# Kernel tuning notes

Measured on AMD Instinct MI355X. Metric: run time of the kernel, lower is better.

## Reference

```python
import jax, jax.numpy as jnp
import numpy as np

K = 64
P = 13               # int(1 + 0.2 * K), module default
KP = K + P - 1       # truncation degree of the polynomial
N_S = 2048
N_C = 10000
NEG = -1e9           # finite stand-in for -inf (log of zero coefficient); keeps vjp NaN-free


def setup_inputs() -> dict:
    key = jax.random.key(0)
    x = jax.random.normal(key, (N_S, N_C), dtype=jnp.float32)
    return {"x": x}


def _log_esp(x, kp):
    """Log elementary symmetric polynomials of exp(x) along the class axis.

    x: (n_s, n_c). Returns L of shape (kp+1, n_s) with
    L[j, s] = log sigma_j(exp(x[s, :])), exactly the truncated log-domain
    polynomial product prod_i (1 + exp(x_i) t) that the torch module computes
    via divide-and-conquer.
    """
    n_s, n_c = x.shape
    # carry: log-coefficients of the partial product, degrees 0..kp
    init = jnp.full((kp + 1, n_s), NEG, dtype=x.dtype).at[0].set(0.0)
    pad = jnp.full((1, n_s), NEG, dtype=x.dtype)

    def step(L, xi):
        # multiply partial polynomial by (1 + exp(xi) t), truncated at degree kp
        shifted = jnp.concatenate([pad, L[:-1] + xi[None, :]], axis=0)
        return jnp.logaddexp(L, shifted), None

    L, _ = jax.lax.scan(step, init, x.T)  # scan over n_c classes
    return L


def reference(x):
    coeff = _log_esp(x, KP)          # (kp+1, n_s)
    return coeff[K - 1:K + 1]        # (2, n_s): log sigma_{k-1}, log sigma_k
```

## Files before the change

### kernel.cpp

```cpp
#include <hip/hip_runtime.h>


#define NS 2048
#define NC 10000
#define KSEL 64

__device__ __forceinline__ float4 ld4(const float* p) { return *(const float4*)p; }

__global__ __launch_bounds__(256, 4)
void logesp_kernel(const float* __restrict__ x, float* __restrict__ out) {
  __shared__ float RA[1280];
  __shared__ float RB[896];
  __shared__ float scLog[32];
  __shared__ float red[8];

  const int t  = threadIdx.x;
  const int wv = t >> 6;
  const int s  = blockIdx.x;

  float c0 = 1.f, c1 = 0.f, c2 = 0.f, c3 = 0.f, c4 = 0.f, c5 = 0.f, c6 = 0.f;
  float sw = 0.f;
  const float4* xv = (const float4*)(x + (size_t)s * NC);

#pragma unroll
  for (int it = 0; it < 9; ++it) {
    const float4 v = xv[t + it * 256];
#pragma unroll
    for (int q = 0; q < 4; ++q) {
      const float xval = q == 0 ? v.x : q == 1 ? v.y : q == 2 ? v.z : v.w;
      const float wgt = __expf(xval);
      sw += wgt;
      c6 = fmaf(wgt, c5, c6);
      c5 = fmaf(wgt, c4, c5);
      c4 = fmaf(wgt, c3, c4);
      c3 = fmaf(wgt, c2, c3);
      c2 = fmaf(wgt, c1, c2);
      c1 = fmaf(wgt, c0, c1);
    }
  }
  if (t < 196) {
    const float4 v = xv[2304 + t];
#pragma unroll
    for (int q = 0; q < 4; ++q) {
      const float xval = q == 0 ? v.x : q == 1 ? v.y : q == 2 ? v.z : v.w;
      const float wgt = __expf(xval);
      sw += wgt;
      c6 = fmaf(wgt, c5, c6);
      c5 = fmaf(wgt, c4, c5);
      c4 = fmaf(wgt, c3, c4);
      c3 = fmaf(wgt, c2, c3);
      c2 = fmaf(wgt, c1, c2);
      c1 = fmaf(wgt, c0, c1);
    }
  }

#pragma unroll
  for (int m = 1; m < 64; m <<= 1) sw += __shfl_xor(sw, m);
  if ((t & 63) == 0) red[wv] = sw;
  if (t < 32) scLog[t] = 0.f;
  __syncthreads();
  const float wsum = red[0] + red[1] + red[2] + red[3];
  const float tau = __logf(wsum * ((float)(NC - KSEL) / ((float)KSEL * (float)NC)));

  {
    const float f1 = __expf(-tau);
    const float f2 = f1 * f1, f3 = f2 * f1, f4v = f2 * f2, f5 = f4v * f1, f6 = f4v * f2;
    c1 *= f1; c2 *= f2; c3 *= f3; c4 *= f4v; c5 *= f5; c6 *= f6;
  }
  float mx = fmaxf(fmaxf(fmaxf(c0, c1), fmaxf(c2, c3)), fmaxf(fmaxf(c4, c5), c6));
  {
    const float inv = 1.f / mx;
    c0 *= inv; c1 *= inv; c2 *= inv; c3 *= inv; c4 *= inv; c5 *= inv; c6 *= inv;
  }
  {
    float Sr = __logf(mx);
#pragma unroll
    for (int m = 1; m < 64; m <<= 1) Sr += __shfl_xor(Sr, m);
    if ((t & 63) == 0) red[4 + wv] = Sr;
  }

  const float q0 = __shfl_xor(c0, 1), q1 = __shfl_xor(c1, 1), q2 = __shfl_xor(c2, 1),
              q3 = __shfl_xor(c3, 1), q4 = __shfl_xor(c4, 1), q5 = __shfl_xor(c5, 1),
              q6 = __shfl_xor(c6, 1);
  float e0 = c0 * q0;
  float e1 = fmaf(c1, q0, c0 * q1);
  float e2 = fmaf(c2, q0, fmaf(c1, q1, c0 * q2));
  float e3 = fmaf(c3, q0, fmaf(c2, q1, fmaf(c1, q2, c0 * q3)));
  float e4 = fmaf(c4, q0, fmaf(c3, q1, fmaf(c2, q2, fmaf(c1, q3, c0 * q4))));
  float e5 = fmaf(c5, q0, fmaf(c4, q1, fmaf(c3, q2, fmaf(c2, q3, fmaf(c1, q4, c0 * q5)))));
  float e6 = fmaf(c6, q0, fmaf(c5, q1, fmaf(c4, q2, fmaf(c3, q3, fmaf(c2, q4, fmaf(c1, q5, c0 * q6))))));
  float e7 = fmaf(c6, q1, fmaf(c5, q2, fmaf(c4, q3, fmaf(c3, q4, fmaf(c2, q5, c1 * q6)))));

  const float f0 = __shfl_xor(e0, 2), f1 = __shfl_xor(e1, 2), f2 = __shfl_xor(e2, 2),
              f3 = __shfl_xor(e3, 2), f4 = __shfl_xor(e4, 2), f5 = __shfl_xor(e5, 2),
              f6 = __shfl_xor(e6, 2), f7 = __shfl_xor(e7, 2);
  const float g0 = e0 * f0;
  const float g1 = fmaf(e1, f0, e0 * f1);
  const float g2 = fmaf(e2, f0, fmaf(e1, f1, e0 * f2));
  const float g3 = fmaf(e3, f0, fmaf(e2, f1, fmaf(e1, f2, e0 * f3)));
  const float g4 = fmaf(e4, f0, fmaf(e3, f1, fmaf(e2, f2, fmaf(e1, f3, e0 * f4))));
  const float g5 = fmaf(e5, f0, fmaf(e4, f1, fmaf(e3, f2, fmaf(e2, f3, fmaf(e1, f4, e0 * f5)))));
  const float g6 = fmaf(e6, f0, fmaf(e5, f1, fmaf(e4, f2, fmaf(e3, f3, fmaf(e2, f4, fmaf(e1, f5, e0 * f6))))));
  const float g7 = fmaf(e7, f0, fmaf(e6, f1, fmaf(e5, f2, fmaf(e4, f3, fmaf(e3, f4, fmaf(e2, f5, fmaf(e1, f6, e0 * f7)))))));
  const float g8 = fmaf(e7, f1, fmaf(e6, f2, fmaf(e5, f3, fmaf(e4, f4, fmaf(e3, f5, fmaf(e2, f6, e1 * f7))))));
  const float g9 = fmaf(e7, f2, fmaf(e6, f3, fmaf(e5, f4, fmaf(e4, f5, fmaf(e3, f6, e2 * f7)))));
  const float g10 = fmaf(e7, f3, fmaf(e6, f4, fmaf(e5, f5, fmaf(e4, f6, e3 * f7))));
  const float g11 = fmaf(e7, f4, fmaf(e6, f5, fmaf(e5, f6, e4 * f7)));

  if ((t & 3) == 0) {
    float* row = RA + (t >> 2) * 20;
    *(float4*)(row)      = make_float4(0.f, 0.f, 0.f, 0.f);
    *(float4*)(row + 4)  = make_float4(g0, g1, g2, g3);
    *(float4*)(row + 8)  = make_float4(g4, g5, g6, g7);
    *(float4*)(row + 12) = make_float4(g8, g9, g10, g11);
    *(float4*)(row + 16) = make_float4(0.f, 0.f, 0.f, 0.f);
  }
  __syncthreads();

  {
    const int m = t >> 3, r = t & 7;
    const float* A = RA + (2 * m) * 20;
    const float* B = RA + (2 * m + 1) * 20;
    float a0 = 0.f, a1 = 0.f, a2 = 0.f, a3 = 0.f;
    if (r < 4) {
      const int j0 = 4 * r;
      const int imax = (j0 + 3 < 12) ? j0 + 3 : 12;
      for (int i0 = 0; i0 <= imax; i0 += 4) {
        const float4 a4 = ld4(A + 4 + i0);
        const float4 bl = ld4(B + j0 - i0);
        const float4 bh = ld4(B + 4 + j0 - i0);
        a0 = fmaf(a4.x, bh.x, a0); a1 = fmaf(a4.x, bh.y, a1); a2 = fmaf(a4.x, bh.z, a2); a3 = fmaf(a4.x, bh.w, a3);
        a0 = fmaf(a4.y, bl.w, a0); a1 = fmaf(a4.y, bh.x, a1); a2 = fmaf(a4.y, bh.y, a2); a3 = fmaf(a4.y, bh.z, a3);
        a0 = fmaf(a4.z, bl.z, a0); a1 = fmaf(a4.z, bl.w, a1); a2 = fmaf(a4.z, bh.x, a2); a3 = fmaf(a4.z, bh.y, a3);
        a0 = fmaf(a4.w, bl.y, a0); a1 = fmaf(a4.w, bl.z, a1); a2 = fmaf(a4.w, bl.w, a2); a3 = fmaf(a4.w, bh.x, a3);
      }
    }
    float m2 = fmaxf(fmaxf(a0, a1), fmaxf(a2, a3));
    m2 = fmaxf(m2, __shfl_xor(m2, 1)); m2 = fmaxf(m2, __shfl_xor(m2, 2)); m2 = fmaxf(m2, __shfl_xor(m2, 4));
    const float inv = 1.f / m2;
    float* o = RB + m * 28;
    if (r < 4) *(float4*)(o + 4 + 4 * r) = make_float4(a0 * inv, a1 * inv, a2 * inv, a3 * inv);
    if (r == 4) *(float4*)(o) = make_float4(0.f, 0.f, 0.f, 0.f);
    if (r == 5) *(float4*)(o + 20) = make_float4(0.f, 0.f, 0.f, 0.f);
    if (r == 0) scLog[m] += __logf(m2);
  }
  __syncthreads();

  {
    const int m = t >> 4, r = t & 15;
    const float* A = RB + (2 * m) * 28;
    const float* B = RB + (2 * m + 1) * 28;
    float a0 = 0.f, a1 = 0.f, a2 = 0.f, a3 = 0.f;
    if (r < 5) {
      const int j0 = 4 * r;
      const int imax = (j0 + 3 < 16) ? j0 + 3 : 16;
      for (int i0 = 0; i0 <= imax; i0 += 4) {
        const float4 a4 = ld4(A + 4 + i0);
        const float4 bl = ld4(B + j0 - i0);
        const float4 bh = ld4(B + 4 + j0 - i0);
        a0 = fmaf(a4.x, bh.x, a0); a1 = fmaf(a4.x, bh.y, a1); a2 = fmaf(a4.x, bh.z, a2); a3 = fmaf(a4.x, bh.w, a3);
        a0 = fmaf(a4.y, bl.w, a0); a1 = fmaf(a4.y, bh.x, a1); a2 = fmaf(a4.y, bh.y, a2); a3 = fmaf(a4.y, bh.z, a3);
        a0 = fmaf(a4.z, bl.z, a0); a1 = fmaf(a4.z, bl.w, a1); a2 = fmaf(a4.z, bh.x, a2); a3 = fmaf(a4.z, bh.y, a3);
        a0 = fmaf(a4.w, bl.y, a0); a1 = fmaf(a4.w, bl.z, a1); a2 = fmaf(a4.w, bl.w, a2); a3 = fmaf(a4.w, bh.x, a3);
      }
    }
    float m2 = fmaxf(fmaxf(a0, a1), fmaxf(a2, a3));
    m2 = fmaxf(m2, __shfl_xor(m2, 1)); m2 = fmaxf(m2, __shfl_xor(m2, 2));
    m2 = fmaxf(m2, __shfl_xor(m2, 4)); m2 = fmaxf(m2, __shfl_xor(m2, 8));
    const float inv = 1.f / m2;
    float* o = RA + m * 52;
    if (r < 5) *(float4*)(o + 20 + 4 * r) = make_float4(a0 * inv, a1 * inv, a2 * inv, a3 * inv);
    if (r >= 5 && r < 10) *(float4*)(o + 4 * (r - 5)) = make_float4(0.f, 0.f, 0.f, 0.f);
    if (r >= 10 && r < 13) *(float4*)(o + 40 + 4 * (r - 10)) = make_float4(0.f, 0.f, 0.f, 0.f);
    if (r == 0) scLog[m] += __logf(m2);
  }
  __syncthreads();

  {
    const int half = (t >> 5) & 1;
    const int m = 2 * wv + half;
    const int p = t & 31;
    const float* A = RA + (2 * m) * 52 + 20;
    const float* B = RA + (2 * m + 1) * 52 + 20;
    float acc = 0.f;
#pragma unroll
    for (int i0 = 0; i0 < 20; i0 += 4) {
      const float4 a4 = ld4(A + i0);
      acc = fmaf(a4.x, B[p - i0], acc);
      acc = fmaf(a4.y, B[p - i0 - 1], acc);
      acc = fmaf(a4.z, B[p - i0 - 2], acc);
      acc = fmaf(a4.w, B[p - i0 - 3], acc);
    }
    float m2 = acc;
    m2 = fmaxf(m2, __shfl_xor(m2, 1)); m2 = fmaxf(m2, __shfl_xor(m2, 2));
    m2 = fmaxf(m2, __shfl_xor(m2, 4)); m2 = fmaxf(m2, __shfl_xor(m2, 8));
    m2 = fmaxf(m2, __shfl_xor(m2, 16));
    const float inv = 1.f / m2;
    float* o = RB + m * 84;
    o[32 + p] = acc * inv;
    if (p < 8) *(float4*)(o + 4 * p) = make_float4(0.f, 0.f, 0.f, 0.f);
    if (p >= 8 && p < 13) *(float4*)(o + 64 + 4 * (p - 8)) = make_float4(0.f, 0.f, 0.f, 0.f);
    if (p == 0) scLog[m] += __logf(m2);
  }
  __syncthreads();

  {
    const int p = t & 63;
    const float* A = RB + (2 * wv) * 84 + 32;
    const float* B = RB + (2 * wv + 1) * 84 + 32;
    float acc = 0.f;
    if (p < 48) {
#pragma unroll
      for (int i0 = 0; i0 < 32; i0 += 4) {
        const float4 a4 = ld4(A + i0);
        acc = fmaf(a4.x, B[p - i0], acc);
        acc = fmaf(a4.y, B[p - i0 - 1], acc);
        acc = fmaf(a4.z, B[p - i0 - 2], acc);
        acc = fmaf(a4.w, B[p - i0 - 3], acc);
      }
    }
    float m2 = acc;
#pragma unroll
    for (int msk = 1; msk < 64; msk <<= 1) m2 = fmaxf(m2, __shfl_xor(m2, msk));
    const float inv = 1.f / m2;
    float* o = RA + wv * 116;
    if (p < 48) o[48 + p] = acc * inv;
    if (p >= 48 && p < 60) *(float4*)(o + 4 * (p - 48)) = make_float4(0.f, 0.f, 0.f, 0.f);
    if (p >= 60) *(float4*)(o + 96 + 4 * (p - 60)) = make_float4(0.f, 0.f, 0.f, 0.f);
    if (p == 59) *(float4*)(o + 112) = make_float4(0.f, 0.f, 0.f, 0.f);
    if (p == 0) scLog[wv] += __logf(m2);
  }
  __syncthreads();

  if (t < 128) {
    const int p = t & 63;
    const float* A = RA + (2 * wv) * 116 + 48;
    const float* B = RA + (2 * wv + 1) * 116 + 48;
    float acc = 0.f;
#pragma unroll
    for (int i0 = 0; i0 < 48; i0 += 4) {
      const float4 a4 = ld4(A + i0);
      acc = fmaf(a4.x, B[p - i0], acc);
      acc = fmaf(a4.y, B[p - i0 - 1], acc);
      acc = fmaf(a4.z, B[p - i0 - 2], acc);
      acc = fmaf(a4.w, B[p - i0 - 3], acc);
    }
    float c64 = (p < 48) ? A[p] * B[64 - p] : 0.f;
#pragma unroll
    for (int msk = 1; msk < 64; msk <<= 1) c64 += __shfl_xor(c64, msk);
    float m2 = fmaxf(acc, c64);
#pragma unroll
    for (int msk = 1; msk < 64; msk <<= 1) m2 = fmaxf(m2, __shfl_xor(m2, msk));
    const float inv = 1.f / m2;
    float* o = RB + wv * 76;
    o[4 + p] = acc * inv;
    if (p == 0) { o[68] = c64 * inv; scLog[wv] += __logf(m2); }
    if (p == 1) *(float4*)(o) = make_float4(0.f, 0.f, 0.f, 0.f);
  }
  __syncthreads();

  if (t < 64) {
    const float* A = RB + 4;
    const float* B = RB + 76 + 4;
    const float a = A[t];
    float v63 = a * B[63 - t];
    float v64 = a * B[64 - t];
    float ee = (t < 32) ? scLog[t] : 0.f;
#pragma unroll
    for (int msk = 1; msk < 64; msk <<= 1) {
      v63 += __shfl_xor(v63, msk);
      v64 += __shfl_xor(v64, msk);
      ee  += __shfl_xor(ee, msk);
    }
    if (t == 0) {
      v64 = fmaf(A[64], B[0], v64);
      const float Ssum = red[4] + red[5] + red[6] + red[7] + ee;
      out[s]      = __logf(v63) + Ssum + 63.f * tau;
      out[NS + s] = __logf(v64) + Ssum + 64.f * tau;
    }
  }
}

extern "C" void kernel_launch(void* const* d_in, const int* in_sizes, int n_in,
                              void* d_out, int out_size, void* d_ws, size_t ws_size,
                              hipStream_t stream) {
  const float* x = (const float*)d_in[0];
  float* out = (float*)d_out;
  (void)in_sizes; (void)n_in; (void)d_ws; (void)ws_size; (void)out_size;
  logesp_kernel<<<NS, 256, 0, stream>>>(x, out);
}
```

Before: 32.28 us.

## Drop block barriers in the tree merge by keeping each level wave-local

Restructures the polynomial-product tree so the first four merge levels each read and write only data owned by the same wavefront. This lets the __syncthreads between those levels be removed. Every level gets its own shared buffer with padded rows and a per-level scLog slot, and the convolutions become scalar-unrolled loops instead of float4 blocked ones. Global loads are all issued up front into a register buffer, with the tail padded by -1e30 instead of a branch, and launch bounds go from 4 to 5 blocks per CU. Risks are higher register pressure from the buffered loads and some extra scalar LDS reads.

```diff
diff --git a/kernel.cpp b/kernel.cpp
--- a/kernel.cpp
+++ b/kernel.cpp
@@ -5,59 +5,50 @@
 #define NC 10000
 #define KSEL 64
 
-__device__ __forceinline__ float4 ld4(const float* p) { return *(const float4*)p; }
-
-__global__ __launch_bounds__(256, 4)
+__global__ __launch_bounds__(256, 5)
 void logesp_kernel(const float* __restrict__ x, float* __restrict__ out) {
-  __shared__ float RA[1280];
-  __shared__ float RB[896];
-  __shared__ float scLog[32];
+  __shared__ float W2[64 * 28];
+  __shared__ float W3[32 * 37];
+  __shared__ float W4[16 * 53];
+  __shared__ float W5[8 * 77];
+  __shared__ float W6[4 * 109];
+  __shared__ float W7[2 * 70];
+  __shared__ float scLog[64];
   __shared__ float red[8];
 
   const int t  = threadIdx.x;
   const int wv = t >> 6;
   const int s  = blockIdx.x;
 
+  const float4* xv = (const float4*)(x + (size_t)s * NC);
+  float4 buf[10];
+#pragma unroll
+  for (int it = 0; it < 9; ++it) buf[it] = xv[t + it * 256];
+  buf[9] = make_float4(-1e30f, -1e30f, -1e30f, -1e30f);
+  if (t < 196) buf[9] = xv[2304 + t];
+
   float c0 = 1.f, c1 = 0.f, c2 = 0.f, c3 = 0.f, c4 = 0.f, c5 = 0.f, c6 = 0.f;
   float sw = 0.f;
-  const float4* xv = (const float4*)(x + (size_t)s * NC);
-
-#pragma unroll
-  for (int it = 0; it < 9; ++it) {
-    const float4 v = xv[t + it * 256];
+#pragma unroll
+  for (int it = 0; it < 10; ++it) {
+    const float4 v = buf[it];
 #pragma unroll
     for (int q = 0; q < 4; ++q) {
       const float xval = q == 0 ? v.x : q == 1 ? v.y : q == 2 ? v.z : v.w;
-      const float wgt = __expf(xval);
-      sw += wgt;
-      c6 = fmaf(wgt, c5, c6);
-      c5 = fmaf(wgt, c4, c5);
-      c4 = fmaf(wgt, c3, c4);
-      c3 = fmaf(wgt, c2, c3);
-      c2 = fmaf(wgt, c1, c2);
-      c1 = fmaf(wgt, c0, c1);
-    }
-  }
-  if (t < 196) {
-    const float4 v = xv[2304 + t];
-#pragma unroll
-    for (int q = 0; q < 4; ++q) {
-      const float xval = q == 0 ? v.x : q == 1 ? v.y : q == 2 ? v.z : v.w;
-      const float wgt = __expf(xval);
-      sw += wgt;
-      c6 = fmaf(wgt, c5, c6);
-      c5 = fmaf(wgt, c4, c5);
-      c4 = fmaf(wgt, c3, c4);
-      c3 = fmaf(wgt, c2, c3);
-      c2 = fmaf(wgt, c1, c2);
-      c1 = fmaf(wgt, c0, c1);
+      const float w = __expf(xval);
+      sw += w;
+      c6 = fmaf(w, c5, c6);
+      c5 = fmaf(w, c4, c5);
+      c4 = fmaf(w, c3, c4);
+      c3 = fmaf(w, c2, c3);
+      c2 = fmaf(w, c1, c2);
+      c1 = fmaf(w, c0, c1);
     }
   }
 
 #pragma unroll
   for (int m = 1; m < 64; m <<= 1) sw += __shfl_xor(sw, m);
   if ((t & 63) == 0) red[wv] = sw;
-  if (t < 32) scLog[t] = 0.f;
   __syncthreads();
   const float wsum = red[0] + red[1] + red[2] + red[3];
   const float tau = __logf(wsum * ((float)(NC - KSEL) / ((float)KSEL * (float)NC)));
@@ -67,12 +58,10 @@
     const float f2 = f1 * f1, f3 = f2 * f1, f4v = f2 * f2, f5 = f4v * f1, f6 = f4v * f2;
     c1 *= f1; c2 *= f2; c3 *= f3; c4 *= f4v; c5 *= f5; c6 *= f6;
   }
-  float mx = fmaxf(fmaxf(fmaxf(c0, c1), fmaxf(c2, c3)), fmaxf(fmaxf(c4, c5), c6));
-  {
-    const float inv = 1.f / mx;
-    c0 *= inv; c1 *= inv; c2 *= inv; c3 *= inv; c4 *= inv; c5 *= inv; c6 *= inv;
-  }
-  {
+  {
+    const float mx = fmaxf(fmaxf(fmaxf(c0, c1), fmaxf(c2, c3)), fmaxf(fmaxf(c4, c5), c6));
+    const float invm = 1.f / mx;
+    c0 *= invm; c1 *= invm; c2 *= invm; c3 *= invm; c4 *= invm; c5 *= invm; c6 *= invm;
     float Sr = __logf(mx);
 #pragma unroll
     for (int m = 1; m < 64; m <<= 1) Sr += __shfl_xor(Sr, m);
@@ -82,14 +71,14 @@
   const float q0 = __shfl_xor(c0, 1), q1 = __shfl_xor(c1, 1), q2 = __shfl_xor(c2, 1),
               q3 = __shfl_xor(c3, 1), q4 = __shfl_xor(c4, 1), q5 = __shfl_xor(c5, 1),
               q6 = __shfl_xor(c6, 1);
-  float e0 = c0 * q0;
-  float e1 = fmaf(c1, q0, c0 * q1);
-  float e2 = fmaf(c2, q0, fmaf(c1, q1, c0 * q2));
-  float e3 = fmaf(c3, q0, fmaf(c2, q1, fmaf(c1, q2, c0 * q3)));
-  float e4 = fmaf(c4, q0, fmaf(c3, q1, fmaf(c2, q2, fmaf(c1, q3, c0 * q4))));
-  float e5 = fmaf(c5, q0, fmaf(c4, q1, fmaf(c3, q2, fmaf(c2, q3, fmaf(c1, q4, c0 * q5)))));
-  float e6 = fmaf(c6, q0, fmaf(c5, q1, fmaf(c4, q2, fmaf(c3, q3, fmaf(c2, q4, fmaf(c1, q5, c0 * q6))))));
-  float e7 = fmaf(c6, q1, fmaf(c5, q2, fmaf(c4, q3, fmaf(c3, q4, fmaf(c2, q5, c1 * q6)))));
+  const float e0 = c0 * q0;
+  const float e1 = fmaf(c1, q0, c0 * q1);
+  const float e2 = fmaf(c2, q0, fmaf(c1, q1, c0 * q2));
+  const float e3 = fmaf(c3, q0, fmaf(c2, q1, fmaf(c1, q2, c0 * q3)));
+  const float e4 = fmaf(c4, q0, fmaf(c3, q1, fmaf(c2, q2, fmaf(c1, q3, c0 * q4))));
+  const float e5 = fmaf(c5, q0, fmaf(c4, q1, fmaf(c3, q2, fmaf(c2, q3, fmaf(c1, q4, c0 * q5)))));
+  const float e6 = fmaf(c6, q0, fmaf(c5, q1, fmaf(c4, q2, fmaf(c3, q3, fmaf(c2, q4, fmaf(c1, q5, c0 * q6))))));
+  const float e7 = fmaf(c6, q1, fmaf(c5, q2, fmaf(c4, q3, fmaf(c3, q4, fmaf(c2, q5, c1 * q6)))));
 
   const float f0 = __shfl_xor(e0, 2), f1 = __shfl_xor(e1, 2), f2 = __shfl_xor(e2, 2),
               f3 = __shfl_xor(e3, 2), f4 = __shfl_xor(e4, 2), f5 = __shfl_xor(e5, 2),
@@ -108,164 +97,144 @@
   const float g11 = fmaf(e7, f4, fmaf(e6, f5, fmaf(e5, f6, e4 * f7)));
 
   if ((t & 3) == 0) {
-    float* row = RA + (t >> 2) * 20;
+    float* row = W2 + (t >> 2) * 28;
     *(float4*)(row)      = make_float4(0.f, 0.f, 0.f, 0.f);
-    *(float4*)(row + 4)  = make_float4(g0, g1, g2, g3);
-    *(float4*)(row + 8)  = make_float4(g4, g5, g6, g7);
-    *(float4*)(row + 12) = make_float4(g8, g9, g10, g11);
-    *(float4*)(row + 16) = make_float4(0.f, 0.f, 0.f, 0.f);
-  }
-  __syncthreads();
+    *(float4*)(row + 4)  = make_float4(0.f, 0.f, 0.f, 0.f);
+    *(float4*)(row + 8)  = make_float4(0.f, 0.f, 0.f, g0);
+    *(float4*)(row + 12) = make_float4(g1, g2, g3, g4);
+    *(float4*)(row + 16) = make_float4(g5, g6, g7, g8);
+    *(float4*)(row + 20) = make_float4(g9, g10, g11, 0.f);
+    *(float4*)(row + 24) = make_float4(0.f, 0.f, 0.f, 0.f);
+  }
 
   {
     const int m = t >> 3, r = t & 7;
-    const float* A = RA + (2 * m) * 20;
-    const float* B = RA + (2 * m + 1) * 20;
-    float a0 = 0.f, a1 = 0.f, a2 = 0.f, a3 = 0.f;
-    if (r < 4) {
-      const int j0 = 4 * r;
-      const int imax = (j0 + 3 < 12) ? j0 + 3 : 12;
-      for (int i0 = 0; i0 <= imax; i0 += 4) {
-        const float4 a4 = ld4(A + 4 + i0);
-        const float4 bl = ld4(B + j0 - i0);
-        const float4 bh = ld4(B + 4 + j0 - i0);
-        a0 = fmaf(a4.x, bh.x, a0); a1 = fmaf(a4.x, bh.y, a1); a2 = fmaf(a4.x, bh.z, a2); a3 = fmaf(a4.x, bh.w, a3);
-        a0 = fmaf(a4.y, bl.w, a0); a1 = fmaf(a4.y, bh.x, a1); a2 = fmaf(a4.y, bh.y, a2); a3 = fmaf(a4.y, bh.z, a3);
-        a0 = fmaf(a4.z, bl.z, a0); a1 = fmaf(a4.z, bl.w, a1); a2 = fmaf(a4.z, bh.x, a2); a3 = fmaf(a4.z, bh.y, a3);
-        a0 = fmaf(a4.w, bl.y, a0); a1 = fmaf(a4.w, bl.z, a1); a2 = fmaf(a4.w, bl.w, a2); a3 = fmaf(a4.w, bh.x, a3);
-      }
-    }
-    float m2 = fmaxf(fmaxf(a0, a1), fmaxf(a2, a3));
-    m2 = fmaxf(m2, __shfl_xor(m2, 1)); m2 = fmaxf(m2, __shfl_xor(m2, 2)); m2 = fmaxf(m2, __shfl_xor(m2, 4));
-    const float inv = 1.f / m2;
-    float* o = RB + m * 28;
-    if (r < 4) *(float4*)(o + 4 + 4 * r) = make_float4(a0 * inv, a1 * inv, a2 * inv, a3 * inv);
-    if (r == 4) *(float4*)(o) = make_float4(0.f, 0.f, 0.f, 0.f);
-    if (r == 5) *(float4*)(o + 20) = make_float4(0.f, 0.f, 0.f, 0.f);
-    if (r == 0) scLog[m] += __logf(m2);
-  }
-  __syncthreads();
+    const float* A = W2 + (2 * m) * 28;
+    const float* B = W2 + (2 * m + 1) * 28;
+    float o0 = 0.f, o1 = 0.f, o2 = 0.f;
+#pragma unroll
+    for (int i = 0; i <= 11; ++i) {
+      const float ai = A[11 + i];
+      o0 = fmaf(ai, B[11 + r - i], o0);
+      o1 = fmaf(ai, B[19 + r - i], o1);
+      o2 = fmaf(ai, B[27 - i], o2);
+    }
+    float mx = fmaxf(fmaxf(o0, o1), o2);
+    mx = fmaxf(mx, __shfl_xor(mx, 1));
+    mx = fmaxf(mx, __shfl_xor(mx, 2));
+    mx = fmaxf(mx, __shfl_xor(mx, 4));
+    const float inv = 1.f / mx;
+    float* O = W3 + m * 37;
+    O[16 + r] = o0 * inv;
+    O[24 + r] = o1 * inv;
+    if (r == 0) { O[32] = o2 * inv; scLog[m] = __logf(mx); }
+    O[r] = 0.f; O[8 + r] = 0.f;
+    if (r < 4) O[33 + r] = 0.f;
+  }
 
   {
     const int m = t >> 4, r = t & 15;
-    const float* A = RB + (2 * m) * 28;
-    const float* B = RB + (2 * m + 1) * 28;
-    float a0 = 0.f, a1 = 0.f, a2 = 0.f, a3 = 0.f;
-    if (r < 5) {
-      const int j0 = 4 * r;
-      const int imax = (j0 + 3 < 16) ? j0 + 3 : 16;
-      for (int i0 = 0; i0 <= imax; i0 += 4) {
-        const float4 a4 = ld4(A + 4 + i0);
-        const float4 bl = ld4(B + j0 - i0);
-        const float4 bh = ld4(B + 4 + j0 - i0);
-        a0 = fmaf(a4.x, bh.x, a0); a1 = fmaf(a4.x, bh.y, a1); a2 = fmaf(a4.x, bh.z, a2); a3 = fmaf(a4.x, bh.w, a3);
-        a0 = fmaf(a4.y, bl.w, a0); a1 = fmaf(a4.y, bh.x, a1); a2 = fmaf(a4.y, bh.y, a2); a3 = fmaf(a4.y, bh.z, a3);
-        a0 = fmaf(a4.z, bl.z, a0); a1 = fmaf(a4.z, bl.w, a1); a2 = fmaf(a4.z, bh.x, a2); a3 = fmaf(a4.z, bh.y, a3);
-        a0 = fmaf(a4.w, bl.y, a0); a1 = fmaf(a4.w, bl.z, a1); a2 = fmaf(a4.w, bl.w, a2); a3 = fmaf(a4.w, bh.x, a3);
-      }
-    }
-    float m2 = fmaxf(fmaxf(a0, a1), fmaxf(a2, a3));
-    m2 = fmaxf(m2, __shfl_xor(m2, 1)); m2 = fmaxf(m2, __shfl_xor(m2, 2));
-    m2 = fmaxf(m2, __shfl_xor(m2, 4)); m2 = fmaxf(m2, __shfl_xor(m2, 8));
-    const float inv = 1.f / m2;
-    float* o = RA + m * 52;
-    if (r < 5) *(float4*)(o + 20 + 4 * r) = make_float4(a0 * inv, a1 * inv, a2 * inv, a3 * inv);
-    if (r >= 5 && r < 10) *(float4*)(o + 4 * (r - 5)) = make_float4(0.f, 0.f, 0.f, 0.f);
-    if (r >= 10 && r < 13) *(float4*)(o + 40 + 4 * (r - 10)) = make_float4(0.f, 0.f, 0.f, 0.f);
-    if (r == 0) scLog[m] += __logf(m2);
-  }
-  __syncthreads();
-
-  {
-    const int half = (t >> 5) & 1;
-    const int m = 2 * wv + half;
-    const int p = t & 31;
-    const float* A = RA + (2 * m) * 52 + 20;
-    const float* B = RA + (2 * m + 1) * 52 + 20;
-    float acc = 0.f;
-#pragma unroll
-    for (int i0 = 0; i0 < 20; i0 += 4) {
-      const float4 a4 = ld4(A + i0);
-      acc = fmaf(a4.x, B[p - i0], acc);
-      acc = fmaf(a4.y, B[p - i0 - 1], acc);
-      acc = fmaf(a4.z, B[p - i0 - 2], acc);
-      acc = fmaf(a4.w, B[p - i0 - 3], acc);
-    }
-    float m2 = acc;
-    m2 = fmaxf(m2, __shfl_xor(m2, 1)); m2 = fmaxf(m2, __shfl_xor(m2, 2));
-    m2 = fmaxf(m2, __shfl_xor(m2, 4)); m2 = fmaxf(m2, __shfl_xor(m2, 8));
-    m2 = fmaxf(m2, __shfl_xor(m2, 16));
-    const float inv = 1.f / m2;
-    float* o = RB + m * 84;
-    o[32 + p] = acc * inv;
-    if (p < 8) *(float4*)(o + 4 * p) = make_float4(0.f, 0.f, 0.f, 0.f);
-    if (p >= 8 && p < 13) *(float4*)(o + 64 + 4 * (p - 8)) = make_float4(0.f, 0.f, 0.f, 0.f);
-    if (p == 0) scLog[m] += __logf(m2);
-  }
-  __syncthreads();
+    const float* A = W3 + (2 * m) * 37;
+    const float* B = W3 + (2 * m + 1) * 37;
+    float o0 = 0.f, o1 = 0.f;
+#pragma unroll
+    for (int i = 0; i <= 16; ++i) {
+      const float ai = A[16 + i];
+      o0 = fmaf(ai, B[16 + r - i], o0);
+      o1 = fmaf(ai, B[32 + r - i], o1);
+    }
+    if (r >= 5) o1 = 0.f;
+    float mx = fmaxf(o0, o1);
+    mx = fmaxf(mx, __shfl_xor(mx, 1));
+    mx = fmaxf(mx, __shfl_xor(mx, 2));
+    mx = fmaxf(mx, __shfl_xor(mx, 4));
+    mx = fmaxf(mx, __shfl_xor(mx, 8));
+    const float inv = 1.f / mx;
+    float* O = W4 + m * 53;
+    O[20 + r] = o0 * inv;
+    if (r < 5) O[36 + r] = o1 * inv;
+    if (r == 0) scLog[32 + m] = __logf(mx);
+    O[r] = 0.f;
+    if (r < 4) O[16 + r] = 0.f;
+    if (r < 12) O[41 + r] = 0.f;
+  }
+
+  {
+    const int m = t >> 5, p = t & 31;
+    const float* A = W4 + (2 * m) * 53;
+    const float* B = W4 + (2 * m + 1) * 53;
+    float o0 = 0.f, o1 = 0.f;
+#pragma unroll
+    for (int i = 0; i <= 20; ++i) {
+      const float ai = A[20 + i];
+      o0 = fmaf(ai, B[20 + p - i], o0);
+      o1 = fmaf(ai, B[52 - i], o1);
+    }
+    float mx = fmaxf(o0, o1);
+    mx = fmaxf(mx, __shfl_xor(mx, 1));
+    mx = fmaxf(mx, __shfl_xor(mx, 2));
+    mx = fmaxf(mx, __shfl_xor(mx, 4));
+    mx = fmaxf(mx, __shfl_xor(mx, 8));
+    mx = fmaxf(mx, __shfl_xor(mx, 16));
+    const float inv = 1.f / mx;
+    float* O = W5 + m * 77;
+    O[32 + p] = o0 * inv;
+    if (p == 0) { O[64] = o1 * inv; scLog[48 + m] = __logf(mx); }
+    O[p] = 0.f;
+    if (p < 12) O[65 + p] = 0.f;
+  }
 
   {
     const int p = t & 63;
-    const float* A = RB + (2 * wv) * 84 + 32;
-    const float* B = RB + (2 * wv + 1) * 84 + 32;
-    float acc = 0.f;
-    if (p < 48) {
-#pragma unroll
-      for (int i0 = 0; i0 < 32; i0 += 4) {
-        const float4 a4 = ld4(A + i0);
-        acc = fmaf(a4.x, B[p - i0], acc);
-        acc = fmaf(a4.y, B[p - i0 - 1], acc);
-        acc = fmaf(a4.z, B[p - i0 - 2], acc);
-        acc = fmaf(a4.w, B[p - i0 - 3], acc);
-      }
-    }
-    float m2 = acc;
-#pragma unroll
-    for (int msk = 1; msk < 64; msk <<= 1) m2 = fmaxf(m2, __shfl_xor(m2, msk));
-    const float inv = 1.f / m2;
-    float* o = RA + wv * 116;
-    if (p < 48) o[48 + p] = acc * inv;
-    if (p >= 48 && p < 60) *(float4*)(o + 4 * (p - 48)) = make_float4(0.f, 0.f, 0.f, 0.f);
-    if (p >= 60) *(float4*)(o + 96 + 4 * (p - 60)) = make_float4(0.f, 0.f, 0.f, 0.f);
-    if (p == 59) *(float4*)(o + 112) = make_float4(0.f, 0.f, 0.f, 0.f);
-    if (p == 0) scLog[wv] += __logf(m2);
+    const float* A = W5 + (2 * wv) * 77;
+    const float* B = W5 + (2 * wv + 1) * 77;
+    float o0 = 0.f;
+#pragma unroll
+    for (int i = 0; i <= 32; ++i) {
+      const float ai = A[32 + i];
+      o0 = fmaf(ai, B[32 + p - i], o0);
+    }
+    if (p >= 45) o0 = 0.f;
+    float mx = o0;
+#pragma unroll
+    for (int msk = 1; msk < 64; msk <<= 1) mx = fmaxf(mx, __shfl_xor(mx, msk));
+    const float inv = 1.f / mx;
+    float* O = W6 + wv * 109;
+    if (p < 45) O[44 + p] = o0 * inv;
+    if (p == 0) scLog[56 + wv] = __logf(mx);
+    if (p < 44) O[p] = 0.f;
+    if (p < 20) O[89 + p] = 0.f;
   }
   __syncthreads();
 
   if (t < 128) {
     const int p = t & 63;
-    const float* A = RA + (2 * wv) * 116 + 48;
-    const float* B = RA + (2 * wv + 1) * 116 + 48;
-    float acc = 0.f;
-#pragma unroll
-    for (int i0 = 0; i0 < 48; i0 += 4) {
-      const float4 a4 = ld4(A + i0);
-      acc = fmaf(a4.x, B[p - i0], acc);
-      acc = fmaf(a4.y, B[p - i0 - 1], acc);
-      acc = fmaf(a4.z, B[p - i0 - 2], acc);
-      acc = fmaf(a4.w, B[p - i0 - 3], acc);
-    }
-    float c64 = (p < 48) ? A[p] * B[64 - p] : 0.f;
-#pragma unroll
-    for (int msk = 1; msk < 64; msk <<= 1) c64 += __shfl_xor(c64, msk);
-    float m2 = fmaxf(acc, c64);
-#pragma unroll
-    for (int msk = 1; msk < 64; msk <<= 1) m2 = fmaxf(m2, __shfl_xor(m2, msk));
-    const float inv = 1.f / m2;
-    float* o = RB + wv * 76;
-    o[4 + p] = acc * inv;
-    if (p == 0) { o[68] = c64 * inv; scLog[wv] += __logf(m2); }
-    if (p == 1) *(float4*)(o) = make_float4(0.f, 0.f, 0.f, 0.f);
+    const float* A = W6 + (2 * wv) * 109;
+    const float* B = W6 + (2 * wv + 1) * 109;
+    float o0 = 0.f, o1 = 0.f;
+#pragma unroll
+    for (int i = 0; i <= 44; ++i) {
+      const float ai = A[44 + i];
+      o0 = fmaf(ai, B[44 + p - i], o0);
+      o1 = fmaf(ai, B[108 - i], o1);
+    }
+    float mx = fmaxf(o0, o1);
+#pragma unroll
+    for (int msk = 1; msk < 64; msk <<= 1) mx = fmaxf(mx, __shfl_xor(mx, msk));
+    const float inv = 1.f / mx;
+    float* O = W7 + wv * 70;
+    O[p] = o0 * inv;
+    if (p == 0) { O[64] = o1 * inv; scLog[60 + wv] = __logf(mx); }
   }
   __syncthreads();
 
   if (t < 64) {
-    const float* A = RB + 4;
-    const float* B = RB + 76 + 4;
+    const float* A = W7;
+    const float* B = W7 + 70;
     const float a = A[t];
     float v63 = a * B[63 - t];
     float v64 = a * B[64 - t];
-    float ee = (t < 32) ? scLog[t] : 0.f;
+    float ee = (t < 62) ? scLog[t] : 0.f;
 #pragma unroll
     for (int msk = 1; msk < 64; msk <<= 1) {
       v63 += __shfl_xor(v63, msk);
```

Measured after the change: 45.72 us. 1.42x slower.
